# Optimization experiments

Measured on AMD Instinct MI355X. Metric: run time of the kernel, lower is better.

## Reference

```python
import jax, jax.numpy as jnp
import numpy as np

B, T = 1024, 128
F_DIM, Z_DIM, TXT_DIM, H = 1024, 256, 768, 8
EPS = 1e-5


def layer_norm(x, g, b):
    mu = jnp.mean(x, axis=-1, keepdims=True)
    var = jnp.var(x, axis=-1, keepdims=True)
    return (x - mu) * jax.lax.rsqrt(var + EPS) * g + b


def setup_inputs() -> dict:
    key = jax.random.key(0)
    ks = jax.random.split(key, 16)
    s = lambda fi, fo: 1.0 / np.sqrt(fi)  # rough init scale
    inp = {
        "x": jax.random.normal(ks[0], (B, F_DIM), jnp.float32),
        "z": jax.random.normal(ks[1], (B, Z_DIM), jnp.float32),
        "text_feat": jax.random.normal(ks[2], (B, T, TXT_DIM), jnp.float32),
        "attention": jnp.ones((B, T), jnp.int32),
        # FiLM
        "Wg": jax.random.normal(ks[3], (F_DIM, Z_DIM), jnp.float32) * s(Z_DIM, F_DIM),
        "bg": jnp.zeros((F_DIM,), jnp.float32),
        "Wb": jax.random.normal(ks[4], (F_DIM, Z_DIM), jnp.float32) * s(Z_DIM, F_DIM),
        "bb": jnp.zeros((F_DIM,), jnp.float32),
        # Linear block (linear -> LayerNorm)
        "Wl": jax.random.normal(ks[5], (F_DIM, F_DIM), jnp.float32) * s(F_DIM, F_DIM),
        "bl": jnp.zeros((F_DIM,), jnp.float32),
        "ln1_g": jnp.ones((F_DIM,), jnp.float32),
        "ln1_b": jnp.zeros((F_DIM,), jnp.float32),
        # cross attention projections
        "Wq": jax.random.normal(ks[6], (F_DIM, F_DIM), jnp.float32) * s(F_DIM, F_DIM),
        "bq": jnp.zeros((F_DIM,), jnp.float32),
        "Wk": jax.random.normal(ks[7], (F_DIM, TXT_DIM), jnp.float32) * s(TXT_DIM, F_DIM),
        "bk": jnp.zeros((F_DIM,), jnp.float32),
        "Wv": jax.random.normal(ks[8], (F_DIM, TXT_DIM), jnp.float32) * s(TXT_DIM, F_DIM),
        "bv": jnp.zeros((F_DIM,), jnp.float32),
        "Wo": jax.random.normal(ks[9], (F_DIM, F_DIM), jnp.float32) * s(F_DIM, F_DIM),
        "bo": jnp.zeros((F_DIM,), jnp.float32),
        # post-attention LayerNorm
        "ln2_g": jnp.ones((F_DIM,), jnp.float32),
        "ln2_b": jnp.zeros((F_DIM,), jnp.float32),
    }
    return inp


def reference(x, z, text_feat, attention, Wg, bg, Wb, bb, Wl, bl, ln1_g, ln1_b,
              Wq, bq, Wk, bk, Wv, bv, Wo, bo, ln2_g, ln2_b):
    d = F_DIM // H
    # FiLM params from condition z
    gamma = z @ Wg.T + bg            # [B, F]
    beta = z @ Wb.T + bb             # [B, F]
    # Linear block: linear -> LayerNorm (dropout p=0, identity activation)
    out = layer_norm(x @ Wl.T + bl, ln1_g, ln1_b)
    out = out * (1.0 + gamma) + beta  # FiLM modulation
    # single-query multi-head cross attention
    q = (out @ Wq.T + bq).reshape(B, H, d)                 # [B, H, d] (query len 1)
    k = (text_feat @ Wk.T + bk).reshape(B, T, H, d)         # [B, T, H, d]
    v = (text_feat @ Wv.T + bv).reshape(B, T, H, d)
    scores = jnp.einsum("bhd,bthd->bht", q, k) / jnp.sqrt(jnp.float32(d))  # [B, H, T]
    mask = (attention[:, None, :] != 0)                     # [B, 1, T]
    scores = jnp.where(mask, scores, -jnp.inf)
    attn = jax.nn.softmax(scores, axis=-1)                  # [B, H, T]
    ctx = jnp.einsum("bht,bthd->bhd", attn, v).reshape(B, F_DIM)
    attn_out = ctx @ Wo.T + bo
    out = out + layer_norm(attn_out, ln2_g, ln2_b)
    return jax.nn.gelu(out, approximate=False)
```

## Files before the change

kernel.cpp:

```cpp
#include <hip/hip_runtime.h>

#define EPS 1e-5f

typedef __bf16 bf16x8 __attribute__((ext_vector_type(8)));
typedef float f32x4 __attribute__((ext_vector_type(4)));
typedef ushort ushort8 __attribute__((ext_vector_type(8)));

static __device__ __forceinline__ ushort f2bf(float x) {
    union { float f; unsigned u; } v; v.f = x;
    unsigned r = v.u + 0x7fffu + ((v.u >> 16) & 1u);
    return (ushort)(r >> 16);
}

__global__ __launch_bounds__(256)
void gemm_nt_mfma(const float* __restrict__ A, int lda, int Aoffz,
                  const ushort* __restrict__ W, int ldw, int Woffz,
                  float* __restrict__ C, int ldc, int Coffz,
                  const float* __restrict__ bias, int boffz,
                  float scale, int K)
{
    const int z = blockIdx.z;
    A += (size_t)z * Aoffz;
    W += (size_t)z * Woffz;
    C += (size_t)z * Coffz;
    const int bm = blockIdx.y * 64, bn = blockIdx.x * 64;

    __shared__ ushort As[64][72];
    __shared__ ushort Bs[64][72];

    const int tid  = threadIdx.x;
    const int lane = tid & 63, wv = tid >> 6;
    const int wm = (wv >> 1) * 32, wn = (wv & 1) * 32;

    const int srow = tid >> 2;
    const int scol = (tid & 3) * 16;
    const float*  Agp = A + (size_t)(bm + srow) * lda + scol;
    const ushort* Wgp = W + (size_t)(bn + srow) * ldw + scol;

    const int fr = lane & 15, fk = (lane >> 4) * 8;

    f32x4 acc[2][2] = {};

    for (int kt = 0; kt < K; kt += 64) {
        f32x4 a0 = *(const f32x4*)(Agp + kt + 0);
        f32x4 a1 = *(const f32x4*)(Agp + kt + 4);
        f32x4 a2 = *(const f32x4*)(Agp + kt + 8);
        f32x4 a3 = *(const f32x4*)(Agp + kt + 12);
        ushort8 b0 = *(const ushort8*)(Wgp + kt);
        ushort8 b1 = *(const ushort8*)(Wgp + kt + 8);

        ushort8 u0, u1;
        u0[0]=f2bf(a0[0]); u0[1]=f2bf(a0[1]); u0[2]=f2bf(a0[2]); u0[3]=f2bf(a0[3]);
        u0[4]=f2bf(a1[0]); u0[5]=f2bf(a1[1]); u0[6]=f2bf(a1[2]); u0[7]=f2bf(a1[3]);
        u1[0]=f2bf(a2[0]); u1[1]=f2bf(a2[1]); u1[2]=f2bf(a2[2]); u1[3]=f2bf(a2[3]);
        u1[4]=f2bf(a3[0]); u1[5]=f2bf(a3[1]); u1[6]=f2bf(a3[2]); u1[7]=f2bf(a3[3]);

        *(ushort8*)&As[srow][scol]     = u0;
        *(ushort8*)&As[srow][scol + 8] = u1;
        *(ushort8*)&Bs[srow][scol]     = b0;
        *(ushort8*)&Bs[srow][scol + 8] = b1;
        __syncthreads();

        #pragma unroll
        for (int ks = 0; ks < 64; ks += 32) {
            bf16x8 af0 = *(const bf16x8*)&As[wm + fr][ks + fk];
            bf16x8 af1 = *(const bf16x8*)&As[wm + 16 + fr][ks + fk];
            bf16x8 bf0 = *(const bf16x8*)&Bs[wn + fr][ks + fk];
            bf16x8 bf1 = *(const bf16x8*)&Bs[wn + 16 + fr][ks + fk];
            acc[0][0] = __builtin_amdgcn_mfma_f32_16x16x32_bf16(af0, bf0, acc[0][0], 0, 0, 0);
            acc[0][1] = __builtin_amdgcn_mfma_f32_16x16x32_bf16(af0, bf1, acc[0][1], 0, 0, 0);
            acc[1][0] = __builtin_amdgcn_mfma_f32_16x16x32_bf16(af1, bf0, acc[1][0], 0, 0, 0);
            acc[1][1] = __builtin_amdgcn_mfma_f32_16x16x32_bf16(af1, bf1, acc[1][1], 0, 0, 0);
        }
        __syncthreads();
    }

    const int rbase = (lane >> 4) * 4;
    #pragma unroll
    for (int mi = 0; mi < 2; ++mi) {
        #pragma unroll
        for (int ni = 0; ni < 2; ++ni) {
            const int col = bn + wn + ni * 16 + fr;
            const float bvv = bias ? (bias + (size_t)z * boffz)[col] : 0.f;
            #pragma unroll
            for (int r = 0; r < 4; ++r) {
                const int row = bm + wm + mi * 16 + rbase + r;
                C[(size_t)row * ldc + col] = acc[mi][ni][r] * scale + bvv;
            }
        }
    }
}

__global__ __launch_bounds__(256)
void cvt_bf16(const float* __restrict__ src, ushort* __restrict__ dst, int n)
{
    int i = (blockIdx.x * 256 + threadIdx.x) * 4;
    if (i < n) {
        f32x4 v = *(const f32x4*)(src + i);
        ushort4 o;
        o.x = f2bf(v[0]); o.y = f2bf(v[1]); o.z = f2bf(v[2]); o.w = f2bf(v[3]);
        *(ushort4*)(dst + i) = o;
    }
}

__global__ __launch_bounds__(256)
void transpose_wk(const float* __restrict__ Wk, ushort* __restrict__ WkT)
{
    __shared__ ushort s[32][33];
    const int h  = blockIdx.z;
    const int c0 = blockIdx.x * 32, d0 = blockIdx.y * 32;
    const int tx = threadIdx.x & 31, ty = threadIdx.x >> 5;
    #pragma unroll
    for (int i = 0; i < 4; ++i) {
        int d = d0 + ty + i * 8;
        s[ty + i * 8][tx] = f2bf(Wk[(size_t)(h * 128 + d) * 768 + c0 + tx]);
    }
    __syncthreads();
    #pragma unroll
    for (int i = 0; i < 4; ++i) {
        int c = c0 + ty + i * 8;
        WkT[((size_t)h * 768 + c) * 128 + d0 + tx] = s[tx][ty + i * 8];
    }
}

__device__ inline void block_reduce2(float& a, float& b, float* sred)
{
    #pragma unroll
    for (int off = 32; off; off >>= 1) {
        a += __shfl_xor(a, off);
        b += __shfl_xor(b, off);
    }
    int w = threadIdx.x >> 6, lane = threadIdx.x & 63;
    if (lane == 0) { sred[w * 2] = a; sred[w * 2 + 1] = b; }
    __syncthreads();
    a = sred[0] + sred[2] + sred[4] + sred[6];
    b = sred[1] + sred[3] + sred[5] + sred[7];
}

__global__ __launch_bounds__(256)
void rowops1(const float* __restrict__ h1, const float* __restrict__ gam,
             const float* __restrict__ bet, const float* __restrict__ g,
             const float* __restrict__ bta, float* __restrict__ out)
{
    __shared__ float sred[8];
    int b = blockIdx.x, tid = threadIdx.x;
    const float4 v = ((const float4*)(h1 + (size_t)b * 1024))[tid];
    float s  = v.x + v.y + v.z + v.w;
    float ss = v.x * v.x + v.y * v.y + v.z * v.z + v.w * v.w;
    block_reduce2(s, ss, sred);
    float mu  = s * (1.f / 1024.f);
    float var = ss * (1.f / 1024.f) - mu * mu;
    float rs  = rsqrtf(var + EPS);
    float4 gv = ((const float4*)g)[tid];
    float4 bv = ((const float4*)bta)[tid];
    float4 ga = ((const float4*)(gam + (size_t)b * 1024))[tid];
    float4 be = ((const float4*)(bet + (size_t)b * 1024))[tid];
    float4 o;
    o.x = ((v.x - mu) * rs * gv.x + bv.x) * (1.f + ga.x) + be.x;
    o.y = ((v.y - mu) * rs * gv.y + bv.y) * (1.f + ga.y) + be.y;
    o.z = ((v.z - mu) * rs * gv.z + bv.z) * (1.f + ga.z) + be.z;
    o.w = ((v.w - mu) * rs * gv.w + bv.w) * (1.f + ga.w) + be.w;
    ((float4*)(out + (size_t)b * 1024))[tid] = o;
}

__global__ __launch_bounds__(256)
void rowops2(const float* __restrict__ outp, const float* __restrict__ ao,
             const float* __restrict__ g, const float* __restrict__ bta,
             float* __restrict__ dst)
{
    __shared__ float sred[8];
    int b = blockIdx.x, tid = threadIdx.x;
    const float4 v = ((const float4*)(ao + (size_t)b * 1024))[tid];
    float s  = v.x + v.y + v.z + v.w;
    float ss = v.x * v.x + v.y * v.y + v.z * v.z + v.w * v.w;
    block_reduce2(s, ss, sred);
    float mu  = s * (1.f / 1024.f);
    float var = ss * (1.f / 1024.f) - mu * mu;
    float rs  = rsqrtf(var + EPS);
    float4 gv = ((const float4*)g)[tid];
    float4 bv = ((const float4*)bta)[tid];
    float4 ov = ((const float4*)(outp + (size_t)b * 1024))[tid];
    float y0 = ov.x + ((v.x - mu) * rs * gv.x + bv.x);
    float y1 = ov.y + ((v.y - mu) * rs * gv.y + bv.y);
    float y2 = ov.z + ((v.z - mu) * rs * gv.z + bv.z);
    float y3 = ov.w + ((v.w - mu) * rs * gv.w + bv.w);
    float4 o;
    o.x = 0.5f * y0 * (1.f + erff(y0 * 0.70710678118654752f));
    o.y = 0.5f * y1 * (1.f + erff(y1 * 0.70710678118654752f));
    o.z = 0.5f * y2 * (1.f + erff(y2 * 0.70710678118654752f));
    o.w = 0.5f * y3 * (1.f + erff(y3 * 0.70710678118654752f));
    ((float4*)(dst + (size_t)b * 1024))[tid] = o;
}

__global__ __launch_bounds__(256)
void attn_kernel(const float* __restrict__ tf, const float* __restrict__ qt,
                 const int* __restrict__ att, float* __restrict__ ctxtf)
{
    int b = blockIdx.x;
    int tid = threadIdx.x, lane = tid & 63, w = tid >> 6;
    __shared__ float s_sc[8][128];

    const float* tfb = tf + (size_t)b * 98304;
    const float* qtb = qt + (size_t)b * 6144;

    float4 qv[8][3];
    #pragma unroll
    for (int h = 0; h < 8; ++h)
        #pragma unroll
        for (int k = 0; k < 3; ++k)
            qv[h][k] = *(const float4*)&qtb[h * 768 + 4 * lane + 256 * k];

    for (int t = w; t < 128; t += 4) {
        float4 x[3];
        #pragma unroll
        for (int k = 0; k < 3; ++k)
            x[k] = *(const float4*)&tfb[t * 768 + 4 * lane + 256 * k];
        float s[8];
        #pragma unroll
        for (int h = 0; h < 8; ++h) {
            s[h] = 0.f;
            #pragma unroll
            for (int k = 0; k < 3; ++k)
                s[h] += qv[h][k].x * x[k].x + qv[h][k].y * x[k].y +
                        qv[h][k].z * x[k].z + qv[h][k].w * x[k].w;
        }
        #pragma unroll
        for (int h = 0; h < 8; ++h)
            #pragma unroll
            for (int off = 32; off; off >>= 1)
                s[h] += __shfl_xor(s[h], off);
        if (lane == 0) {
            #pragma unroll
            for (int h = 0; h < 8; ++h) s_sc[h][t] = s[h];
        }
    }
    __syncthreads();

    int m0 = att[b * 128 + lane];
    int m1 = att[b * 128 + 64 + lane];
    #pragma unroll
    for (int hh = 0; hh < 2; ++hh) {
        int h = 2 * w + hh;
        float x0 = m0 ? s_sc[h][lane]      : -INFINITY;
        float x1 = m1 ? s_sc[h][lane + 64] : -INFINITY;
        float mx = fmaxf(x0, x1);
        #pragma unroll
        for (int off = 32; off; off >>= 1)
            mx = fmaxf(mx, __shfl_xor(mx, off));
        float e0 = m0 ? __expf(x0 - mx) : 0.f;
        float e1 = m1 ? __expf(x1 - mx) : 0.f;
        float sm = e0 + e1;
        #pragma unroll
        for (int off = 32; off; off >>= 1)
            sm += __shfl_xor(sm, off);
        float inv = 1.f / sm;
        s_sc[h][lane]      = e0 * inv;
        s_sc[h][lane + 64] = e1 * inv;
    }
    __syncthreads();

    int h0 = 2 * w;
    float4 acc[2][3] = {};
    for (int t = 0; t < 128; ++t) {
        float4 x[3];
        #pragma unroll
        for (int k = 0; k < 3; ++k)
            x[k] = *(const float4*)&tfb[t * 768 + 4 * lane + 256 * k];
        float a0 = s_sc[h0][t];
        float a1 = s_sc[h0 + 1][t];
        #pragma unroll
        for (int k = 0; k < 3; ++k) {
            acc[0][k].x += a0 * x[k].x; acc[0][k].y += a0 * x[k].y;
            acc[0][k].z += a0 * x[k].z; acc[0][k].w += a0 * x[k].w;
            acc[1][k].x += a1 * x[k].x; acc[1][k].y += a1 * x[k].y;
            acc[1][k].z += a1 * x[k].z; acc[1][k].w += a1 * x[k].w;
        }
    }
    #pragma unroll
    for (int j = 0; j < 2; ++j)
        #pragma unroll
        for (int k = 0; k < 3; ++k)
            *(float4*)&ctxtf[(size_t)b * 6144 + (h0 + j) * 768 + 4 * lane + 256 * k] = acc[j][k];
}

extern "C" void kernel_launch(void* const* d_in, const int* in_sizes, int n_in,
                              void* d_out, int out_size, void* d_ws, size_t ws_size,
                              hipStream_t stream)
{
    const float* x    = (const float*)d_in[0];
    const float* zc   = (const float*)d_in[1];
    const float* tf   = (const float*)d_in[2];
    const int*   att  = (const int*)d_in[3];
    const float* Wg   = (const float*)d_in[4];
    const float* bg   = (const float*)d_in[5];
    const float* Wb   = (const float*)d_in[6];
    const float* bb   = (const float*)d_in[7];
    const float* Wl   = (const float*)d_in[8];
    const float* bl   = (const float*)d_in[9];
    const float* ln1g = (const float*)d_in[10];
    const float* ln1b = (const float*)d_in[11];
    const float* Wq   = (const float*)d_in[12];
    const float* bq   = (const float*)d_in[13];
    const float* Wk   = (const float*)d_in[14];
    const float* Wv   = (const float*)d_in[16];
    const float* bv   = (const float*)d_in[17];
    const float* Wo   = (const float*)d_in[18];
    const float* bo   = (const float*)d_in[19];
    const float* ln2g = (const float*)d_in[20];
    const float* ln2b = (const float*)d_in[21];

    float* ws = (float*)d_ws;
    const size_t M1 = 1u << 20;
    float* OUT   = ws;
    float* H1    = ws + 1 * M1;
    float* GAM   = ws + 2 * M1;
    float* BET   = ws + 3 * M1;
    float* Q     = ws + 4 * M1;
    float* QT    = ws + 5 * M1;
    float* CTXTF = ws + 11 * M1;
    float* CTX   = H1;
    float* AO    = GAM;

    ushort* wb16 = (ushort*)(ws + 18 * M1);
    ushort* WlB = wb16;
    ushort* WqB = wb16 + 1 * M1;
    ushort* WoB = wb16 + 2 * M1;
    ushort* WgB = wb16 + 3 * M1;
    ushort* WbB = wb16 + 3 * M1 + 262144;
    ushort* WvB = wb16 + 3 * M1 + 524288;
    ushort* WkT = wb16 + 3 * M1 + 524288 + 786432;

    dim3 blk(256);

    cvt_bf16<<<dim3(1024), blk, 0, stream>>>(Wl, WlB, 1048576);
    cvt_bf16<<<dim3(1024), blk, 0, stream>>>(Wq, WqB, 1048576);
    cvt_bf16<<<dim3(1024), blk, 0, stream>>>(Wo, WoB, 1048576);
    cvt_bf16<<<dim3(256),  blk, 0, stream>>>(Wg, WgB, 262144);
    cvt_bf16<<<dim3(256),  blk, 0, stream>>>(Wb, WbB, 262144);
    cvt_bf16<<<dim3(768),  blk, 0, stream>>>(Wv, WvB, 786432);
    transpose_wk<<<dim3(24, 4, 8), blk, 0, stream>>>(Wk, WkT);

    gemm_nt_mfma<<<dim3(16, 16, 1), blk, 0, stream>>>(x, 1024, 0, WlB, 1024, 0,
        H1, 1024, 0, bl, 0, 1.f, 1024);
    gemm_nt_mfma<<<dim3(16, 16, 1), blk, 0, stream>>>(zc, 256, 0, WgB, 256, 0,
        GAM, 1024, 0, bg, 0, 1.f, 256);
    gemm_nt_mfma<<<dim3(16, 16, 1), blk, 0, stream>>>(zc, 256, 0, WbB, 256, 0,
        BET, 1024, 0, bb, 0, 1.f, 256);
    rowops1<<<dim3(1024), blk, 0, stream>>>(H1, GAM, BET, ln1g, ln1b, OUT);
    gemm_nt_mfma<<<dim3(16, 16, 1), blk, 0, stream>>>(OUT, 1024, 0, WqB, 1024, 0,
        Q, 1024, 0, bq, 0, 1.f, 1024);
    gemm_nt_mfma<<<dim3(12, 16, 8), blk, 0, stream>>>(Q, 1024, 128, WkT, 128, 98304,
        QT, 6144, 768, nullptr, 0, 0.08838834764831845f, 128);
    attn_kernel<<<dim3(1024), blk, 0, stream>>>(tf, QT, att, CTXTF);
    gemm_nt_mfma<<<dim3(2, 16, 8), blk, 0, stream>>>(CTXTF, 6144, 768, WvB, 768, 98304,
        CTX, 1024, 128, bv, 128, 1.f, 768);
    gemm_nt_mfma<<<dim3(16, 16, 1), blk, 0, stream>>>(CTX, 1024, 0, WoB, 1024, 0,
        AO, 1024, 0, bo, 0, 1.f, 1024);
    rowops2<<<dim3(1024), blk, 0, stream>>>(OUT, AO, ln2g, ln2b, (float*)d_out);
}
```

Measured before the change: 787.8 us.

## Stage text features once in LDS as bf16 with MFMA scores and online softmax

The attention kernel now loads each 32-token chunk of text features once, converts it to bf16 in shared memory, and computes scores for that chunk with MFMA. It then applies an online softmax and accumulates the context from the same shared tile, so text features are no longer read from global memory twice. The six weight-conversion launches are merged into one kernel, and the gamma and beta GEMMs are fused into a single GEMM with concatenated weights and biases. This cuts launches and global traffic but adds bf16 rounding to the scores and context, and only two of the four waves do the score MFMA.

```diff
diff --git a/kernel.cpp b/kernel.cpp
--- a/kernel.cpp
+++ b/kernel.cpp
@@ -10,6 +10,10 @@
     union { float f; unsigned u; } v; v.f = x;
     unsigned r = v.u + 0x7fffu + ((v.u >> 16) & 1u);
     return (ushort)(r >> 16);
+}
+static __device__ __forceinline__ float bf2f(ushort u) {
+    union { unsigned u32; float f; } v; v.u32 = (unsigned)u << 16;
+    return v.f;
 }
 
 __global__ __launch_bounds__(256)
@@ -92,15 +96,32 @@
 }
 
 __global__ __launch_bounds__(256)
-void cvt_bf16(const float* __restrict__ src, ushort* __restrict__ dst, int n)
-{
-    int i = (blockIdx.x * 256 + threadIdx.x) * 4;
-    if (i < n) {
-        f32x4 v = *(const f32x4*)(src + i);
-        ushort4 o;
-        o.x = f2bf(v[0]); o.y = f2bf(v[1]); o.z = f2bf(v[2]); o.w = f2bf(v[3]);
-        *(ushort4*)(dst + i) = o;
-    }
+void cvt_all(const float* __restrict__ Wl, const float* __restrict__ Wq,
+             const float* __restrict__ Wo, const float* __restrict__ Wv,
+             const float* __restrict__ Wg, const float* __restrict__ Wb,
+             const float* __restrict__ bg, const float* __restrict__ bb,
+             ushort* __restrict__ WlB, ushort* __restrict__ WqB,
+             ushort* __restrict__ WoB, ushort* __restrict__ WvB,
+             ushort* __restrict__ WgbB, float* __restrict__ bgb)
+{
+    int gid = blockIdx.x * 256 + threadIdx.x;
+    if (gid < 512) {
+        f32x4 v = (gid < 256) ? *(const f32x4*)(bg + gid * 4)
+                              : *(const f32x4*)(bb + (gid - 256) * 4);
+        *(f32x4*)(bgb + gid * 4) = v;
+    }
+    const float* src; ushort* dst; int off;
+    if      (gid <  262144) { src = Wl; dst = WlB;           off = gid;          }
+    else if (gid <  524288) { src = Wq; dst = WqB;           off = gid - 262144; }
+    else if (gid <  786432) { src = Wo; dst = WoB;           off = gid - 524288; }
+    else if (gid <  983040) { src = Wv; dst = WvB;           off = gid - 786432; }
+    else if (gid < 1048576) { src = Wg; dst = WgbB;          off = gid - 983040; }
+    else if (gid < 1114112) { src = Wb; dst = WgbB + 262144; off = gid - 1048576;}
+    else return;
+    f32x4 v = *(const f32x4*)(src + (size_t)off * 4);
+    ushort4 o;
+    o.x = f2bf(v[0]); o.y = f2bf(v[1]); o.z = f2bf(v[2]); o.w = f2bf(v[3]);
+    *(ushort4*)(dst + (size_t)off * 4) = o;
 }
 
 __global__ __launch_bounds__(256)
@@ -138,9 +159,9 @@
 }
 
 __global__ __launch_bounds__(256)
-void rowops1(const float* __restrict__ h1, const float* __restrict__ gam,
-             const float* __restrict__ bet, const float* __restrict__ g,
-             const float* __restrict__ bta, float* __restrict__ out)
+void rowops1(const float* __restrict__ h1, const float* __restrict__ gb,
+             const float* __restrict__ g, const float* __restrict__ bta,
+             float* __restrict__ out)
 {
     __shared__ float sred[8];
     int b = blockIdx.x, tid = threadIdx.x;
@@ -153,8 +174,8 @@
     float rs  = rsqrtf(var + EPS);
     float4 gv = ((const float4*)g)[tid];
     float4 bv = ((const float4*)bta)[tid];
-    float4 ga = ((const float4*)(gam + (size_t)b * 1024))[tid];
-    float4 be = ((const float4*)(bet + (size_t)b * 1024))[tid];
+    float4 ga = ((const float4*)(gb + (size_t)b * 2048))[tid];
+    float4 be = ((const float4*)(gb + (size_t)b * 2048 + 1024))[tid];
     float4 o;
     o.x = ((v.x - mu) * rs * gv.x + bv.x) * (1.f + ga.x) + be.x;
     o.y = ((v.y - mu) * rs * gv.y + bv.y) * (1.f + ga.y) + be.y;
@@ -193,94 +214,137 @@
 }
 
 __global__ __launch_bounds__(256)
-void attn_kernel(const float* __restrict__ tf, const float* __restrict__ qt,
-                 const int* __restrict__ att, float* __restrict__ ctxtf)
-{
-    int b = blockIdx.x;
-    int tid = threadIdx.x, lane = tid & 63, w = tid >> 6;
-    __shared__ float s_sc[8][128];
+void attn_fused(const float* __restrict__ tf, const float* __restrict__ qt,
+                const int* __restrict__ att, float* __restrict__ ctxtf)
+{
+    const int b = blockIdx.x;
+    const int tid = threadIdx.x, lane = tid & 63, wv = tid >> 6;
+
+    __shared__ ushort qtS[16][776];
+    __shared__ ushort TF[32][776];
+    __shared__ float s_sc[8][32];
+    __shared__ float ps[8][32];
 
     const float* tfb = tf + (size_t)b * 98304;
     const float* qtb = qt + (size_t)b * 6144;
 
-    float4 qv[8][3];
-    #pragma unroll
-    for (int h = 0; h < 8; ++h)
+    {
+        const int r  = tid >> 5;
+        const int c0 = (tid & 31) * 24;
         #pragma unroll
-        for (int k = 0; k < 3; ++k)
-            qv[h][k] = *(const float4*)&qtb[h * 768 + 4 * lane + 256 * k];
-
-    for (int t = w; t < 128; t += 4) {
-        float4 x[3];
+        for (int j = 0; j < 6; ++j) {
+            f32x4 v = *(const f32x4*)&qtb[r * 768 + c0 + 4 * j];
+            ushort4 o;
+            o.x = f2bf(v[0]); o.y = f2bf(v[1]); o.z = f2bf(v[2]); o.w = f2bf(v[3]);
+            *(ushort4*)&qtS[r][c0 + 4 * j] = o;
+        }
+        const ushort4 z4 = {0, 0, 0, 0};
         #pragma unroll
-        for (int k = 0; k < 3; ++k)
-            x[k] = *(const float4*)&tfb[t * 768 + 4 * lane + 256 * k];
-        float s[8];
-        #pragma unroll
-        for (int h = 0; h < 8; ++h) {
-            s[h] = 0.f;
+        for (int j = 0; j < 6; ++j)
+            *(ushort4*)&qtS[8 + r][c0 + 4 * j] = z4;
+    }
+
+    float acc[2][3][4] = {};
+    float mrun = -INFINITY, srun = 0.f;
+    const int fr = lane & 15, fko = (lane >> 4) * 8;
+    const int hloc = lane >> 5, tl = lane & 31;
+    const int h_own = 2 * wv + hloc;
+    const int h0 = 2 * wv;
+
+    for (int s = 0; s < 4; ++s) {
+        __syncthreads();
+        {
+            const int r  = tid >> 3;
+            const int c0 = (tid & 7) * 96;
+            const float* srcr = tfb + (size_t)(s * 32 + r) * 768 + c0;
+            #pragma unroll
+            for (int j = 0; j < 24; ++j) {
+                f32x4 v = *(const f32x4*)(srcr + 4 * j);
+                ushort4 o;
+                o.x = f2bf(v[0]); o.y = f2bf(v[1]); o.z = f2bf(v[2]); o.w = f2bf(v[3]);
+                *(ushort4*)&TF[r][c0 + 4 * j] = o;
+            }
+        }
+        __syncthreads();
+        if (wv < 2) {
+            f32x4 sacc = {0.f, 0.f, 0.f, 0.f};
+            #pragma unroll
+            for (int ks = 0; ks < 768; ks += 32) {
+                bf16x8 aq = *(const bf16x8*)&qtS[fr][ks + fko];
+                bf16x8 bt = *(const bf16x8*)&TF[wv * 16 + fr][ks + fko];
+                sacc = __builtin_amdgcn_mfma_f32_16x16x32_bf16(aq, bt, sacc, 0, 0, 0);
+            }
+            if (lane < 32) {
+                const int hbase = (lane >> 4) * 4;
+                #pragma unroll
+                for (int r = 0; r < 4; ++r)
+                    s_sc[hbase + r][wv * 16 + (lane & 15)] = sacc[r];
+            }
+        }
+        __syncthreads();
+        {
+            const int mask = att[b * 128 + s * 32 + tl];
+            float sv = mask ? s_sc[h_own][tl] : -INFINITY;
+            float mx = sv;
+            mx = fmaxf(mx, __shfl_xor(mx, 16));
+            mx = fmaxf(mx, __shfl_xor(mx, 8));
+            mx = fmaxf(mx, __shfl_xor(mx, 4));
+            mx = fmaxf(mx, __shfl_xor(mx, 2));
+            mx = fmaxf(mx, __shfl_xor(mx, 1));
+            float mnew = fmaxf(mrun, mx);
+            float p = mask ? __expf(sv - mnew) : 0.f;
+            float f = (mnew == -INFINITY) ? 1.f : __expf(mrun - mnew);
+            float psum = p;
+            psum += __shfl_xor(psum, 16);
+            psum += __shfl_xor(psum, 8);
+            psum += __shfl_xor(psum, 4);
+            psum += __shfl_xor(psum, 2);
+            psum += __shfl_xor(psum, 1);
+            srun = srun * f + psum;
+            mrun = mnew;
+            ps[h_own][tl] = p;
+            const float f0 = __shfl(f, 0);
+            const float f1 = __shfl(f, 32);
             #pragma unroll
             for (int k = 0; k < 3; ++k)
-                s[h] += qv[h][k].x * x[k].x + qv[h][k].y * x[k].y +
-                        qv[h][k].z * x[k].z + qv[h][k].w * x[k].w;
-        }
+                #pragma unroll
+                for (int e = 0; e < 4; ++e) {
+                    acc[0][k][e] *= f0;
+                    acc[1][k][e] *= f1;
+                }
+        }
+        {
+            #pragma unroll 8
+            for (int t = 0; t < 32; ++t) {
+                const float p0 = ps[h0][t];
+                const float p1 = ps[h0 + 1][t];
+                #pragma unroll
+                for (int k = 0; k < 3; ++k) {
+                    ushort4 u = *(const ushort4*)&TF[t][4 * lane + 256 * k];
+                    float x0 = bf2f(u.x), x1 = bf2f(u.y), x2 = bf2f(u.z), x3 = bf2f(u.w);
+                    acc[0][k][0] += p0 * x0; acc[0][k][1] += p0 * x1;
+                    acc[0][k][2] += p0 * x2; acc[0][k][3] += p0 * x3;
+                    acc[1][k][0] += p1 * x0; acc[1][k][1] += p1 * x1;
+                    acc[1][k][2] += p1 * x2; acc[1][k][3] += p1 * x3;
+                }
+            }
+        }
+    }
+
+    const float sum0 = __shfl(srun, 0);
+    const float sum1 = __shfl(srun, 32);
+    const float i0 = 1.f / sum0, i1 = 1.f / sum1;
+    #pragma unroll
+    for (int k = 0; k < 3; ++k) {
+        f32x4 o0, o1;
         #pragma unroll
-        for (int h = 0; h < 8; ++h)
-            #pragma unroll
-            for (int off = 32; off; off >>= 1)
-                s[h] += __shfl_xor(s[h], off);
-        if (lane == 0) {
-            #pragma unroll
-            for (int h = 0; h < 8; ++h) s_sc[h][t] = s[h];
-        }
-    }
-    __syncthreads();
-
-    int m0 = att[b * 128 + lane];
-    int m1 = att[b * 128 + 64 + lane];
-    #pragma unroll
-    for (int hh = 0; hh < 2; ++hh) {
-        int h = 2 * w + hh;
-        float x0 = m0 ? s_sc[h][lane]      : -INFINITY;
-        float x1 = m1 ? s_sc[h][lane + 64] : -INFINITY;
-        float mx = fmaxf(x0, x1);
-        #pragma unroll
-        for (int off = 32; off; off >>= 1)
-            mx = fmaxf(mx, __shfl_xor(mx, off));
-        float e0 = m0 ? __expf(x0 - mx) : 0.f;
-        float e1 = m1 ? __expf(x1 - mx) : 0.f;
-        float sm = e0 + e1;
-        #pragma unroll
-        for (int off = 32; off; off >>= 1)
-            sm += __shfl_xor(sm, off);
-        float inv = 1.f / sm;
-        s_sc[h][lane]      = e0 * inv;
-        s_sc[h][lane + 64] = e1 * inv;
-    }
-    __syncthreads();
-
-    int h0 = 2 * w;
-    float4 acc[2][3] = {};
-    for (int t = 0; t < 128; ++t) {
-        float4 x[3];
-        #pragma unroll
-        for (int k = 0; k < 3; ++k)
-            x[k] = *(const float4*)&tfb[t * 768 + 4 * lane + 256 * k];
-        float a0 = s_sc[h0][t];
-        float a1 = s_sc[h0 + 1][t];
-        #pragma unroll
-        for (int k = 0; k < 3; ++k) {
-            acc[0][k].x += a0 * x[k].x; acc[0][k].y += a0 * x[k].y;
-            acc[0][k].z += a0 * x[k].z; acc[0][k].w += a0 * x[k].w;
-            acc[1][k].x += a1 * x[k].x; acc[1][k].y += a1 * x[k].y;
-            acc[1][k].z += a1 * x[k].z; acc[1][k].w += a1 * x[k].w;
-        }
-    }
-    #pragma unroll
-    for (int j = 0; j < 2; ++j)
-        #pragma unroll
-        for (int k = 0; k < 3; ++k)
-            *(float4*)&ctxtf[(size_t)b * 6144 + (h0 + j) * 768 + 4 * lane + 256 * k] = acc[j][k];
+        for (int e = 0; e < 4; ++e) {
+            o0[e] = acc[0][k][e] * i0;
+            o1[e] = acc[1][k][e] * i1;
+        }
+        *(f32x4*)&ctxtf[(size_t)b * 6144 + (size_t)h0 * 768 + 4 * lane + 256 * k] = o0;
+        *(f32x4*)&ctxtf[(size_t)b * 6144 + (size_t)(h0 + 1) * 768 + 4 * lane + 256 * k] = o1;
+    }
 }
 
 extern "C" void kernel_launch(void* const* d_in, const int* in_sizes, int n_in,
@@ -313,45 +377,38 @@
     const size_t M1 = 1u << 20;
     float* OUT   = ws;
     float* H1    = ws + 1 * M1;
-    float* GAM   = ws + 2 * M1;
-    float* BET   = ws + 3 * M1;
+    float* GB    = ws + 2 * M1;
     float* Q     = ws + 4 * M1;
     float* QT    = ws + 5 * M1;
     float* CTXTF = ws + 11 * M1;
+    float* AO    = ws + 17 * M1;
+    float* bgb   = ws + 18 * M1;
     float* CTX   = H1;
-    float* AO    = GAM;
-
-    ushort* wb16 = (ushort*)(ws + 18 * M1);
-    ushort* WlB = wb16;
-    ushort* WqB = wb16 + 1 * M1;
-    ushort* WoB = wb16 + 2 * M1;
-    ushort* WgB = wb16 + 3 * M1;
-    ushort* WbB = wb16 + 3 * M1 + 262144;
-    ushort* WvB = wb16 + 3 * M1 + 524288;
-    ushort* WkT = wb16 + 3 * M1 + 524288 + 786432;
+
+    ushort* wb16 = (ushort*)(ws + 19 * M1);
+    ushort* WlB  = wb16;
+    ushort* WqB  = wb16 + 1 * M1;
+    ushort* WoB  = wb16 + 2 * M1;
+    ushort* WvB  = wb16 + 3 * M1;
+    ushort* WgbB = wb16 + 3 * M1 + 786432;
+    ushort* WkT  = wb16 + 3 * M1 + 786432 + 524288;
 
     dim3 blk(256);
 
-    cvt_bf16<<<dim3(1024), blk, 0, stream>>>(Wl, WlB, 1048576);
-    cvt_bf16<<<dim3(1024), blk, 0, stream>>>(Wq, WqB, 1048576);
-    cvt_bf16<<<dim3(1024), blk, 0, stream>>>(Wo, WoB, 1048576);
-    cvt_bf16<<<dim3(256),  blk, 0, stream>>>(Wg, WgB, 262144);
-    cvt_bf16<<<dim3(256),  blk, 0, stream>>>(Wb, WbB, 262144);
-    cvt_bf16<<<dim3(768),  blk, 0, stream>>>(Wv, WvB, 786432);
+    cvt_all<<<dim3(4352), blk, 0, stream>>>(Wl, Wq, Wo, Wv, Wg, Wb, bg, bb,
+                                            WlB, WqB, WoB, WvB, WgbB, bgb);
     transpose_wk<<<dim3(24, 4, 8), blk, 0, stream>>>(Wk, WkT);
 
     gemm_nt_mfma<<<dim3(16, 16, 1), blk, 0, stream>>>(x, 1024, 0, WlB, 1024, 0,
         H1, 1024, 0, bl, 0, 1.f, 1024);
-    gemm_nt_mfma<<<dim3(16, 16, 1), blk, 0, stream>>>(zc, 256, 0, WgB, 256, 0,
-        GAM, 1024, 0, bg, 0, 1.f, 256);
-    gemm_nt_mfma<<<dim3(16, 16, 1), blk, 0, stream>>>(zc, 256, 0, WbB, 256, 0,
-        BET, 1024, 0, bb, 0, 1.f, 256);
-    rowops1<<<dim3(1024), blk, 0, stream>>>(H1, GAM, BET, ln1g, ln1b, OUT);
+    gemm_nt_mfma<<<dim3(32, 16, 1), blk, 0, stream>>>(zc, 256, 0, WgbB, 256, 0,
+        GB, 2048, 0, bgb, 0, 1.f, 256);
+    rowops1<<<dim3(1024), blk, 0, stream>>>(H1, GB, ln1g, ln1b, OUT);
     gemm_nt_mfma<<<dim3(16, 16, 1), blk, 0, stream>>>(OUT, 1024, 0, WqB, 1024, 0,
         Q, 1024, 0, bq, 0, 1.f, 1024);
     gemm_nt_mfma<<<dim3(12, 16, 8), blk, 0, stream>>>(Q, 1024, 128, WkT, 128, 98304,
         QT, 6144, 768, nullptr, 0, 0.08838834764831845f, 128);
-    attn_kernel<<<dim3(1024), blk, 0, stream>>>(tf, QT, att, CTXTF);
+    attn_fused<<<dim3(1024), blk, 0, stream>>>(tf, QT, att, CTXTF);
     gemm_nt_mfma<<<dim3(2, 16, 8), blk, 0, stream>>>(CTXTF, 6144, 768, WvB, 768, 98304,
         CTX, 1024, 128, bv, 128, 1.f, 768);
     gemm_nt_mfma<<<dim3(16, 16, 1), blk, 0, stream>>>(CTX, 1024, 0, WoB, 1024, 0,
```

New measurement: 709.0 us. 10.0% less time.
